# Performance work log

Measured on AMD Instinct MI355X. Metric: run time of the kernel, lower is better.

## Reference

```python
import jax, jax.numpy as jnp
import numpy as np

N_L = 100000   # local nodes
N_V = 1000     # virtual nodes
D_IN = 64
H = 64         # hidden_channels
D_OUT = 32
E_LL = 1000000
E_LV = 100000
E_VV = 50000


def setup_inputs() -> dict:
    key = jax.random.key(0)
    ks = jax.random.split(key, 16)
    s_in = 1.0 / np.sqrt(D_IN)   # fan-in init scale
    s_h = 1.0 / np.sqrt(H)
    return {
        "x_local": jax.random.normal(ks[0], (N_L, D_IN), jnp.float32),
        "x_virtual": jax.random.normal(ks[1], (N_V, D_IN), jnp.float32),
        # GCNConv (local->local): weight + bias
        "W_gcn": jax.random.normal(ks[2], (D_IN, H), jnp.float32) * s_in,
        "b_gcn": jnp.zeros((H,), jnp.float32),
        # SAGEConv (local->virtual): lin_l (neighbor agg, with bias), lin_r (root)
        "Wl_lv": jax.random.normal(ks[3], (D_IN, H), jnp.float32) * s_in,
        "Wr_lv": jax.random.normal(ks[4], (D_IN, H), jnp.float32) * s_in,
        "b_lv": jnp.zeros((H,), jnp.float32),
        # SAGEConv (virtual->virtual)
        "Wl_vv": jax.random.normal(ks[5], (D_IN, H), jnp.float32) * s_in,
        "Wr_vv": jax.random.normal(ks[6], (D_IN, H), jnp.float32) * s_in,
        "b_vv": jnp.zeros((H,), jnp.float32),
        # final Linear(hidden -> dim_out)
        "W_lin": jax.random.normal(ks[7], (H, D_OUT), jnp.float32) * s_h,
        "b_lin": jnp.zeros((D_OUT,), jnp.float32),
        # edge indices
        "edge_ll": jax.random.randint(ks[8], (2, E_LL), 0, N_L),
        "edge_lv_src": jax.random.randint(ks[9], (E_LV,), 0, N_L),
        "edge_lv_dst": jax.random.randint(ks[10], (E_LV,), 0, N_V),
        "edge_vv": jax.random.randint(ks[11], (2, E_VV), 0, N_V),
    }


def _gcn_conv(x, W, b, row, col, n):
    # gcn_norm with add_self_loops=False: deg from dst (col), sym norm
    ones = jnp.ones(row.shape[0], x.dtype)
    deg = jax.ops.segment_sum(ones, col, num_segments=n)
    dinv = jnp.where(deg > 0, jax.lax.rsqrt(jnp.maximum(deg, 1.0)), 0.0)
    norm = dinv[row] * dinv[col]                      # [E]
    h = x @ W                                         # [n,H]
    msg = h[row] * norm[:, None]                      # [E,H] gather
    return jax.ops.segment_sum(msg, col, num_segments=n) + b


def _sage_conv(x_src, x_dst, Wl, Wr, b, src, dst, n_dst):
    # mean aggregation of source features over in-edges
    agg = jax.ops.segment_sum(x_src[src], dst, num_segments=n_dst)
    cnt = jax.ops.segment_sum(jnp.ones(src.shape[0], x_src.dtype), dst,
                              num_segments=n_dst)
    agg = agg / jnp.maximum(cnt, 1.0)[:, None]
    return agg @ Wl + b + x_dst @ Wr


def reference(x_local, x_virtual, W_gcn, b_gcn, Wl_lv, Wr_lv, b_lv,
              Wl_vv, Wr_vv, b_vv, W_lin, b_lin,
              edge_ll, edge_lv_src, edge_lv_dst, edge_vv):
    # HeteroConv layer (sum-aggregate outputs per destination node type)
    out_ll = _gcn_conv(x_local, W_gcn, b_gcn, edge_ll[0], edge_ll[1], N_L)
    out_lv = _sage_conv(x_local, x_virtual, Wl_lv, Wr_lv, b_lv,
                        edge_lv_src, edge_lv_dst, N_V)
    out_vv = _sage_conv(x_virtual, x_virtual, Wl_vv, Wr_vv, b_vv,
                        edge_vv[0], edge_vv[1], N_V)
    h_local = jax.nn.relu(out_ll)
    h_virtual = jax.nn.relu(out_lv + out_vv)  # sum across relations -> relu
    del h_virtual  # only 'local' feeds the final linear head
    return h_local @ W_lin + b_lin
```

## Files before the change

### kernel.cpp

```cpp
#include <hip/hip_runtime.h>

#define N_L 100000
#define N_V 1000
#define D_IN 64
#define HCH 64
#define D_OUT 32
#define E_LL 1000000

#define NCLS 8
#define DST_PER_CLS 12500
#define NBLK1 1024
#define BCAP 256
#define GW 400
#define NSB 32
#define NGSB 256
#define SUBCAP 4608
#define SCSTRIDE 16

#define L2CAP 384
#define L2THR 128
#define BINSUB_BPC 64
#define SLABS (NBLK1 / BINSUB_BPC)

typedef unsigned int uint32;
typedef unsigned long long u64;
typedef __attribute__((ext_vector_type(8))) short bfx8;
typedef __attribute__((ext_vector_type(4))) float f32x4;
typedef __attribute__((ext_vector_type(4))) float fvec4;
typedef __attribute__((ext_vector_type(4))) unsigned short usvec4;

__device__ inline float bf2f(unsigned short u) {
    return __uint_as_float(((uint32)u) << 16);
}
__device__ inline unsigned short f2bf(float f) {
    uint32 u = __float_as_uint(f);
    u = (u + 0x7fffu + ((u >> 16) & 1u)) >> 16;
    return (unsigned short)u;
}
__device__ inline void bar_lds() {
    asm volatile("s_waitcnt lgkmcnt(0)\n\ts_barrier" ::: "memory");
}

__global__ __launch_bounds__(256) void binclass_kernel(
    const int* __restrict__ row, const int* __restrict__ col,
    int* __restrict__ classcnt, uint32* __restrict__ classpairs)
{
    __shared__ uint32 sbin[NCLS][BCAP];
    __shared__ int scnt[NCLS];
    if (threadIdx.x < NCLS) scnt[threadIdx.x] = 0;
    bar_lds();

    const int blk = blockIdx.x;
    const int per = (E_LL + NBLK1 - 1) / NBLK1;
    const int beg = blk * per;
    const int end = (beg + per < E_LL) ? beg + per : E_LL;
    const int lane = threadIdx.x & 63;
    const int wv = threadIdx.x >> 6;

    for (int i0 = beg; i0 < end; i0 += 256) {
        int i = i0 + threadIdx.x;
        if (i < end) {
            int c = col[i];
            int r = row[i];
            int cls = c / DST_PER_CLS;
            uint32 pack = ((uint32)r << 14) | (uint32)(c - cls * DST_PER_CLS);
            u64 act = __ballot(1);
            u64 b0 = __ballot(cls & 1);
            u64 b1 = __ballot(cls & 2);
            u64 b2 = __ballot(cls & 4);
            u64 mask = ((cls & 1) ? b0 : ~b0) & ((cls & 2) ? b1 : ~b1)
                     & ((cls & 4) ? b2 : ~b2) & act;
            int leader = __ffsll(mask) - 1;
            int rank = __popcll(mask & ((1ull << lane) - 1ull));
            int base = 0;
            if (lane == leader) base = atomicAdd(&scnt[cls], __popcll(mask));
            base = __shfl(base, leader);
            int slot = base + rank;
            if (slot < BCAP) sbin[cls][slot] = pack;
        }
    }
    bar_lds();
    for (int b = wv; b < NCLS; b += 4) {
        int cnt = scnt[b]; if (cnt > BCAP) cnt = BCAP;
        uint32* dst = classpairs + ((size_t)b * NBLK1 + blk) * BCAP;
        for (int k = lane; k < cnt; k += 64) dst[k] = sbin[b][k];
        if (lane == 0) classcnt[b * NBLK1 + blk] = cnt;
    }
}

__global__ __launch_bounds__(256) void binsub_kernel(
    const int* __restrict__ classcnt, const uint32* __restrict__ classpairs,
    int* __restrict__ subcur, uint32* __restrict__ subpairs)
{
    __shared__ uint32 sbin[NSB][L2CAP];
    __shared__ int scnt[NSB];
    if (threadIdx.x < NSB) scnt[threadIdx.x] = 0;
    bar_lds();

    const int cls = blockIdx.x / BINSUB_BPC;
    const int chunk = blockIdx.x % BINSUB_BPC;
    const int s0 = chunk * SLABS;
    const int lane = threadIdx.x & 63;
    const int wv = threadIdx.x >> 6;

    for (int s = s0; s < s0 + SLABS; ++s) {
        int len = classcnt[cls * NBLK1 + s];
        const uint32* cp = classpairs + ((size_t)cls * NBLK1 + s) * BCAP;
        if (threadIdx.x < len) {
            uint32 p = cp[threadIdx.x];
            int c_lo = (int)(p & 16383u);
            uint32 r = p >> 14;
            int sb = c_lo / GW;
            uint32 pack = (r << 9) | (uint32)(c_lo - sb * GW);
            u64 act = __ballot(1);
            u64 b0 = __ballot(sb & 1);
            u64 b1 = __ballot(sb & 2);
            u64 b2 = __ballot(sb & 4);
            u64 b3 = __ballot(sb & 8);
            u64 b4 = __ballot(sb & 16);
            u64 mask = ((sb & 1) ? b0 : ~b0) & ((sb & 2) ? b1 : ~b1)
                     & ((sb & 4) ? b2 : ~b2) & ((sb & 8) ? b3 : ~b3)
                     & ((sb & 16) ? b4 : ~b4) & act;
            int leader = __ffsll(mask) - 1;
            int rank = __popcll(mask & ((1ull << lane) - 1ull));
            int base = 0;
            if (lane == leader) base = atomicAdd(&scnt[sb], __popcll(mask));
            base = __shfl(base, leader);
            sbin[sb][base + rank] = pack;
        }
        bar_lds();
        for (int b = wv; b < NSB; b += 4) {
            int cnt = scnt[b];
            if (cnt >= L2THR) {
                int gb;
                int gsb = cls * NSB + b;
                if (lane == 0) gb = atomicAdd(&subcur[gsb * SCSTRIDE], cnt);
                gb = __shfl(gb, 0);
                uint32* dst = subpairs + (size_t)gsb * SUBCAP;
                for (int k = lane; k < cnt; k += 64)
                    if (gb + k < SUBCAP) dst[gb + k] = sbin[b][k];
                if (lane == 0) scnt[b] = 0;
            }
        }
        bar_lds();
    }
    for (int b = wv; b < NSB; b += 4) {
        int cnt = scnt[b];
        if (cnt > 0) {
            int gb;
            int gsb = cls * NSB + b;
            if (lane == 0) gb = atomicAdd(&subcur[gsb * SCSTRIDE], cnt);
            gb = __shfl(gb, 0);
            uint32* dst = subpairs + (size_t)gsb * SUBCAP;
            for (int k = lane; k < cnt; k += 64)
                if (gb + k < SUBCAP) dst[gb + k] = sbin[b][k];
        }
    }
}

__global__ __launch_bounds__(512) void degdinv_kernel(
    const uint32* __restrict__ subpairs, const int* __restrict__ subcur,
    float* __restrict__ dinv)
{
    __shared__ int hcnt[512];
    const int gsb = blockIdx.x;
    const int cls = gsb >> 5;
    const int sb = gsb & 31;
    const int lo = cls * DST_PER_CLS + sb * GW;
    int w = DST_PER_CLS - sb * GW; if (w > GW) w = GW;

    hcnt[threadIdx.x] = 0;
    bar_lds();
    int cnt = subcur[gsb * SCSTRIDE]; if (cnt > SUBCAP) cnt = SUBCAP;
    const uint32* sp = subpairs + (size_t)gsb * SUBCAP;
    for (int i = threadIdx.x; i < cnt; i += 512)
        atomicAdd(&hcnt[sp[i] & 511u], 1);
    bar_lds();
    if (threadIdx.x < w) {
        int d = hcnt[threadIdx.x];
        dinv[lo + threadIdx.x] = (d > 0) ? rsqrtf((float)d) : 0.0f;
    }
}

__global__ void xbconv_kernel(const float* __restrict__ x,
                              const float* __restrict__ dinv,
                              unsigned short* __restrict__ xb) {
    int n4 = N_L * D_IN / 4;
    int idx = blockIdx.x * blockDim.x + threadIdx.x;
    int stride = gridDim.x * blockDim.x;
    for (; idx < n4; idx += stride) {
        fvec4 v = ((const fvec4*)x)[idx];
        float d = dinv[idx >> 4];
        usvec4 o;
        o.x = f2bf(v.x * d);
        o.y = f2bf(v.y * d);
        o.z = f2bf(v.z * d);
        o.w = f2bf(v.w * d);
        ((usvec4*)xb)[idx] = o;
    }
}

__global__ __launch_bounds__(1024) void gather_epi_kernel(
    const unsigned short* __restrict__ xb,
    const uint32* __restrict__ subpairs, const int* __restrict__ subcur,
    const float* __restrict__ Wg, const float* __restrict__ bg,
    const float* __restrict__ Wl, const float* __restrict__ bl,
    float* __restrict__ out)
{
    extern __shared__ char smem[];
    unsigned short* hacc = (unsigned short*)smem;
    unsigned short* hbufp = (unsigned short*)(smem + 57600);
    uint32* sorted = (uint32*)(smem + 94464);
    int* rptr  = (int*)(smem + 112896);
    int* scan2 = (int*)(smem + 114944);
    int* cur   = (int*)(smem + 116992);

    const int gsb = blockIdx.x;
    const int cls = gsb >> 5;
    const int sb = gsb & 31;
    const int lo = cls * DST_PER_CLS + sb * GW;
    int w = DST_PER_CLS - sb * GW; if (w > GW) w = GW;

    const int tid = threadIdx.x;
    const int lane = tid & 63;
    const int wv = tid >> 6;

    int cnt = subcur[gsb * SCSTRIDE]; if (cnt > SUBCAP) cnt = SUBCAP;
    const uint32* sp = subpairs + (size_t)gsb * SUBCAP;

    if (tid < 512) rptr[tid] = 0;
    bar_lds();
    for (int i = tid; i < cnt; i += 1024)
        atomicAdd(&rptr[sp[i] & 511u], 1);
    bar_lds();

    int v = (tid < 512) ? rptr[tid] : 0;
    if (tid < 512) scan2[tid] = v;
    bar_lds();
    for (int ofs = 1; ofs < 512; ofs <<= 1) {
        int add = (tid < 512 && tid >= ofs) ? scan2[tid - ofs] : 0;
        bar_lds();
        if (tid < 512) scan2[tid] += add;
        bar_lds();
    }
    if (tid < 512) {
        int ex = scan2[tid] - v;
        rptr[tid] = ex;
        if (tid < 400) cur[tid] = ex;
    }
    bar_lds();

    for (int i = tid; i < cnt; i += 1024) {
        uint32 p = sp[i];
        int pos = atomicAdd(&cur[p & 511u], 1);
        sorted[pos] = p >> 9;
    }
    bar_lds();

    for (int c = wv; c < w; c += 16) {
        int s = rptr[c], e = rptr[c + 1];
        int cntc = e - s;
        float a0 = 0.f, a1 = 0.f, a2 = 0.f, a3 = 0.f;
        float a4 = 0.f, a5 = 0.f, a6 = 0.f, a7 = 0.f;
        int j = s;
        for (; j + 8 <= e; j += 8) {
            int r0 = sorted[j], r1 = sorted[j + 1];
            int r2 = sorted[j + 2], r3 = sorted[j + 3];
            int r4 = sorted[j + 4], r5 = sorted[j + 5];
            int r6 = sorted[j + 6], r7 = sorted[j + 7];
            a0 += bf2f(xb[(size_t)r0 * D_IN + lane]);
            a1 += bf2f(xb[(size_t)r1 * D_IN + lane]);
            a2 += bf2f(xb[(size_t)r2 * D_IN + lane]);
            a3 += bf2f(xb[(size_t)r3 * D_IN + lane]);
            a4 += bf2f(xb[(size_t)r4 * D_IN + lane]);
            a5 += bf2f(xb[(size_t)r5 * D_IN + lane]);
            a6 += bf2f(xb[(size_t)r6 * D_IN + lane]);
            a7 += bf2f(xb[(size_t)r7 * D_IN + lane]);
        }
        for (; j < e; ++j) {
            int r = sorted[j];
            a0 += bf2f(xb[(size_t)r * D_IN + lane]);
        }
        float dv = (cntc > 0) ? rsqrtf((float)cntc) : 0.0f;
        float s01 = (a0 + a1) + (a2 + a3);
        float s23 = (a4 + a5) + (a6 + a7);
        hacc[c * 72 + lane] = f2bf((s01 + s23) * dv);
    }
    bar_lds();

    const int lm = lane & 15, lg = lane >> 4, kseg = lg * 8;

    bfx8 wg0[4], wg1[4], wl0[2], wl1[2];
    #pragma unroll
    for (int n = 0; n < 4; ++n) {
        #pragma unroll
        for (int jj = 0; jj < 8; ++jj) {
            wg0[n][jj] = (short)f2bf(Wg[(kseg + jj) * HCH + n * 16 + lm]);
            wg1[n][jj] = (short)f2bf(Wg[(32 + kseg + jj) * HCH + n * 16 + lm]);
        }
    }
    #pragma unroll
    for (int n = 0; n < 2; ++n) {
        #pragma unroll
        for (int jj = 0; jj < 8; ++jj) {
            wl0[n][jj] = (short)f2bf(Wl[(kseg + jj) * D_OUT + n * 16 + lm]);
            wl1[n][jj] = (short)f2bf(Wl[(32 + kseg + jj) * D_OUT + n * 16 + lm]);
        }
    }
    float bgv[4], blv[2];
    #pragma unroll
    for (int n = 0; n < 4; ++n) bgv[n] = bg[n * 16 + lm];
    #pragma unroll
    for (int n = 0; n < 2; ++n) blv[n] = bl[n * 16 + lm];

    const int ntile = (w + 15) >> 4;
    for (int t = wv; t < ntile; t += 16) {
        const int m0 = t * 16;
        const int arow = m0 + lm;
        const unsigned short* fr = hacc + arow * 72;
        bfx8 a0 = *(const bfx8*)(fr + kseg);
        bfx8 a1 = *(const bfx8*)(fr + 32 + kseg);

        unsigned short* hb = hbufp + wv * (16 * 72);
        #pragma unroll
        for (int n = 0; n < 4; ++n) {
            f32x4 cacc = {0.0f, 0.0f, 0.0f, 0.0f};
            cacc = __builtin_amdgcn_mfma_f32_16x16x32_bf16(a0, wg0[n], cacc, 0, 0, 0);
            cacc = __builtin_amdgcn_mfma_f32_16x16x32_bf16(a1, wg1[n], cacc, 0, 0, 0);
            #pragma unroll
            for (int i = 0; i < 4; ++i) {
                float h = fmaxf(cacc[i] + bgv[n], 0.0f);
                hb[(lg * 4 + i) * 72 + n * 16 + lm] = f2bf(h);
            }
        }
        bfx8 a20 = *(const bfx8*)(hb + lm * 72 + kseg);
        bfx8 a21 = *(const bfx8*)(hb + lm * 72 + 32 + kseg);

        #pragma unroll
        for (int n2 = 0; n2 < 2; ++n2) {
            f32x4 d = {0.0f, 0.0f, 0.0f, 0.0f};
            d = __builtin_amdgcn_mfma_f32_16x16x32_bf16(a20, wl0[n2], d, 0, 0, 0);
            d = __builtin_amdgcn_mfma_f32_16x16x32_bf16(a21, wl1[n2], d, 0, 0, 0);
            #pragma unroll
            for (int i = 0; i < 4; ++i) {
                int mrow = m0 + lg * 4 + i;
                if (mrow < w)
                    out[(size_t)(lo + mrow) * D_OUT + n2 * 16 + lm] = d[i] + blv[n2];
            }
        }
    }
}

extern "C" void kernel_launch(void* const* d_in, const int* in_sizes, int n_in,
                              void* d_out, int out_size, void* d_ws, size_t ws_size,
                              hipStream_t stream) {
    const float* x_local = (const float*)d_in[0];
    const float* W_gcn   = (const float*)d_in[2];
    const float* b_gcn   = (const float*)d_in[3];
    const float* W_lin   = (const float*)d_in[10];
    const float* b_lin   = (const float*)d_in[11];
    const int*   edge_ll = (const int*)d_in[12];
    const int*   row = edge_ll;
    const int*   col = edge_ll + E_LL;

    char* base = (char*)d_ws;
    int*    subcur     = (int*)(base + 0);
    int*    classcnt   = (int*)(base + 16384);
    float*  dinvp      = (float*)(base + 49152);
    uint32* classpairs = (uint32*)(base + 449536);
    uint32* subpairs   = (uint32*)(base + 8838144);
    unsigned short* xb = (unsigned short*)(base + 13556736);
    float* out = (float*)d_out;

    (void)hipMemsetAsync(base, 0, 16384, stream);

    binclass_kernel<<<NBLK1, 256, 0, stream>>>(row, col, classcnt, classpairs);
    binsub_kernel<<<NCLS * BINSUB_BPC, 256, 0, stream>>>(
        classcnt, classpairs, subcur, subpairs);
    degdinv_kernel<<<NGSB, 512, 0, stream>>>(subpairs, subcur, dinvp);
    xbconv_kernel<<<2048, 256, 0, stream>>>(x_local, dinvp, xb);
    gather_epi_kernel<<<NGSB, 1024, 118592, stream>>>(
        xb, subpairs, subcur, W_gcn, b_gcn, W_lin, b_lin, out);
}
```

Before: 112.4 us.

## Split gather-epilogue into half-bin blocks and reuse precomputed row pointers

The degree kernel now also computes the per-sub-bin exclusive prefix sum and writes it to global memory. The gather-epilogue kernel is split so each 400-node bin is handled by two 512-thread blocks of 200 nodes, using about half the LDS. This drops the in-kernel histogram and scan, and the smaller blocks should improve occupancy and spread work across more CUs. In exchange, each block still scans the whole bin's pair list and keeps only the half it owns, and a new SORTCAP bound can silently drop edges if one half overflows.

```diff
diff --git a/kernel.cpp b/kernel.cpp
--- a/kernel.cpp
+++ b/kernel.cpp
@@ -12,9 +12,11 @@
 #define NBLK1 1024
 #define BCAP 256
 #define GW 400
+#define HW 200
 #define NSB 32
 #define NGSB 256
 #define SUBCAP 4608
+#define SORTCAP 2560
 #define SCSTRIDE 16
 
 #define L2CAP 384
@@ -160,26 +162,37 @@
 
 __global__ __launch_bounds__(512) void degdinv_kernel(
     const uint32* __restrict__ subpairs, const int* __restrict__ subcur,
-    float* __restrict__ dinv)
+    float* __restrict__ dinv, int* __restrict__ rptrg)
 {
     __shared__ int hcnt[512];
+    __shared__ int scn[512];
     const int gsb = blockIdx.x;
     const int cls = gsb >> 5;
     const int sb = gsb & 31;
     const int lo = cls * DST_PER_CLS + sb * GW;
     int w = DST_PER_CLS - sb * GW; if (w > GW) w = GW;
-
-    hcnt[threadIdx.x] = 0;
+    const int tid = threadIdx.x;
+
+    hcnt[tid] = 0;
     bar_lds();
     int cnt = subcur[gsb * SCSTRIDE]; if (cnt > SUBCAP) cnt = SUBCAP;
     const uint32* sp = subpairs + (size_t)gsb * SUBCAP;
-    for (int i = threadIdx.x; i < cnt; i += 512)
+    for (int i = tid; i < cnt; i += 512)
         atomicAdd(&hcnt[sp[i] & 511u], 1);
     bar_lds();
-    if (threadIdx.x < w) {
-        int d = hcnt[threadIdx.x];
-        dinv[lo + threadIdx.x] = (d > 0) ? rsqrtf((float)d) : 0.0f;
-    }
+
+    int v = hcnt[tid];
+    scn[tid] = v;
+    bar_lds();
+    for (int ofs = 1; ofs < 512; ofs <<= 1) {
+        int add = (tid >= ofs) ? scn[tid - ofs] : 0;
+        bar_lds();
+        scn[tid] += add;
+        bar_lds();
+    }
+    rptrg[gsb * 512 + tid] = scn[tid] - v;
+    if (tid < w)
+        dinv[lo + tid] = (v > 0) ? rsqrtf((float)v) : 0.0f;
 }
 
 __global__ void xbconv_kernel(const float* __restrict__ x,
@@ -200,26 +213,30 @@
     }
 }
 
-__global__ __launch_bounds__(1024) void gather_epi_kernel(
+__global__ __launch_bounds__(512) void gather_epi_kernel(
     const unsigned short* __restrict__ xb,
     const uint32* __restrict__ subpairs, const int* __restrict__ subcur,
+    const int* __restrict__ rptrg,
     const float* __restrict__ Wg, const float* __restrict__ bg,
     const float* __restrict__ Wl, const float* __restrict__ bl,
     float* __restrict__ out)
 {
     extern __shared__ char smem[];
-    unsigned short* hacc = (unsigned short*)smem;
-    unsigned short* hbufp = (unsigned short*)(smem + 57600);
-    uint32* sorted = (uint32*)(smem + 94464);
-    int* rptr  = (int*)(smem + 112896);
-    int* scan2 = (int*)(smem + 114944);
-    int* cur   = (int*)(smem + 116992);
-
-    const int gsb = blockIdx.x;
+    unsigned short* hacc  = (unsigned short*)smem;
+    unsigned short* hbufp = (unsigned short*)(smem + 29952);
+    uint32* sorted = (uint32*)(smem + 48384);
+    int* rptr_l = (int*)(smem + 58624);
+    int* cur    = (int*)(smem + 59456);
+
+    const int gsb = blockIdx.x >> 1;
+    const int hb  = blockIdx.x & 1;
     const int cls = gsb >> 5;
-    const int sb = gsb & 31;
-    const int lo = cls * DST_PER_CLS + sb * GW;
-    int w = DST_PER_CLS - sb * GW; if (w > GW) w = GW;
+    const int sb  = gsb & 31;
+    const int lo_bin = cls * DST_PER_CLS + sb * GW;
+    int wbin = DST_PER_CLS - sb * GW; if (wbin > GW) wbin = GW;
+    const int lo_node = hb * HW;
+    int w = wbin - lo_node; if (w > HW) w = HW; if (w < 0) w = 0;
+    const int lo = lo_bin + lo_node;
 
     const int tid = threadIdx.x;
     const int lane = tid & 63;
@@ -227,38 +244,29 @@
 
     int cnt = subcur[gsb * SCSTRIDE]; if (cnt > SUBCAP) cnt = SUBCAP;
     const uint32* sp = subpairs + (size_t)gsb * SUBCAP;
-
-    if (tid < 512) rptr[tid] = 0;
-    bar_lds();
-    for (int i = tid; i < cnt; i += 1024)
-        atomicAdd(&rptr[sp[i] & 511u], 1);
-    bar_lds();
-
-    int v = (tid < 512) ? rptr[tid] : 0;
-    if (tid < 512) scan2[tid] = v;
-    bar_lds();
-    for (int ofs = 1; ofs < 512; ofs <<= 1) {
-        int add = (tid < 512 && tid >= ofs) ? scan2[tid - ofs] : 0;
-        bar_lds();
-        if (tid < 512) scan2[tid] += add;
-        bar_lds();
-    }
-    if (tid < 512) {
-        int ex = scan2[tid] - v;
-        rptr[tid] = ex;
-        if (tid < 400) cur[tid] = ex;
-    }
-    bar_lds();
-
-    for (int i = tid; i < cnt; i += 1024) {
+    const int* rg = rptrg + gsb * 512;
+
+    const int base0 = rg[lo_node];
+    if (tid <= w) {
+        int rl = rg[lo_node + tid] - base0;
+        rptr_l[tid] = rl;
+        if (tid < w) cur[tid] = rl;
+    }
+    bar_lds();
+
+    for (int i = tid; i < cnt; i += 512) {
         uint32 p = sp[i];
-        int pos = atomicAdd(&cur[p & 511u], 1);
-        sorted[pos] = p >> 9;
-    }
-    bar_lds();
-
-    for (int c = wv; c < w; c += 16) {
-        int s = rptr[c], e = rptr[c + 1];
+        int cl = (int)(p & 511u) - lo_node;
+        if (cl >= 0 && cl < w) {
+            int pos = atomicAdd(&cur[cl], 1);
+            if (pos < SORTCAP) sorted[pos] = p >> 9;
+        }
+    }
+    bar_lds();
+
+    for (int c = wv; c < w; c += 8) {
+        int s = rptr_l[c], e = rptr_l[c + 1];
+        if (e > SORTCAP) e = SORTCAP;
         int cntc = e - s;
         float a0 = 0.f, a1 = 0.f, a2 = 0.f, a3 = 0.f;
         float a4 = 0.f, a5 = 0.f, a6 = 0.f, a7 = 0.f;
@@ -288,6 +296,8 @@
     }
     bar_lds();
 
+    if (w == 0) return;
+
     const int lm = lane & 15, lg = lane >> 4, kseg = lg * 8;
 
     bfx8 wg0[4], wg1[4], wl0[2], wl1[2];
@@ -314,14 +324,14 @@
     for (int n = 0; n < 2; ++n) blv[n] = bl[n * 16 + lm];
 
     const int ntile = (w + 15) >> 4;
-    for (int t = wv; t < ntile; t += 16) {
+    for (int t = wv; t < ntile; t += 8) {
         const int m0 = t * 16;
         const int arow = m0 + lm;
         const unsigned short* fr = hacc + arow * 72;
         bfx8 a0 = *(const bfx8*)(fr + kseg);
         bfx8 a1 = *(const bfx8*)(fr + 32 + kseg);
 
-        unsigned short* hb = hbufp + wv * (16 * 72);
+        unsigned short* hbw = hbufp + wv * (16 * 72);
         #pragma unroll
         for (int n = 0; n < 4; ++n) {
             f32x4 cacc = {0.0f, 0.0f, 0.0f, 0.0f};
@@ -330,11 +340,11 @@
             #pragma unroll
             for (int i = 0; i < 4; ++i) {
                 float h = fmaxf(cacc[i] + bgv[n], 0.0f);
-                hb[(lg * 4 + i) * 72 + n * 16 + lm] = f2bf(h);
+                hbw[(lg * 4 + i) * 72 + n * 16 + lm] = f2bf(h);
             }
         }
-        bfx8 a20 = *(const bfx8*)(hb + lm * 72 + kseg);
-        bfx8 a21 = *(const bfx8*)(hb + lm * 72 + 32 + kseg);
+        bfx8 a20 = *(const bfx8*)(hbw + lm * 72 + kseg);
+        bfx8 a21 = *(const bfx8*)(hbw + lm * 72 + 32 + kseg);
 
         #pragma unroll
         for (int n2 = 0; n2 < 2; ++n2) {
@@ -367,9 +377,10 @@
     int*    subcur     = (int*)(base + 0);
     int*    classcnt   = (int*)(base + 16384);
     float*  dinvp      = (float*)(base + 49152);
-    uint32* classpairs = (uint32*)(base + 449536);
-    uint32* subpairs   = (uint32*)(base + 8838144);
-    unsigned short* xb = (unsigned short*)(base + 13556736);
+    int*    rptrg      = (int*)(base + 449536);
+    uint32* classpairs = (uint32*)(base + 973824);
+    uint32* subpairs   = (uint32*)(base + 9362432);
+    unsigned short* xb = (unsigned short*)(base + 14081024);
     float* out = (float*)d_out;
 
     (void)hipMemsetAsync(base, 0, 16384, stream);
@@ -377,8 +388,8 @@
     binclass_kernel<<<NBLK1, 256, 0, stream>>>(row, col, classcnt, classpairs);
     binsub_kernel<<<NCLS * BINSUB_BPC, 256, 0, stream>>>(
         classcnt, classpairs, subcur, subpairs);
-    degdinv_kernel<<<NGSB, 512, 0, stream>>>(subpairs, subcur, dinvp);
+    degdinv_kernel<<<NGSB, 512, 0, stream>>>(subpairs, subcur, dinvp, rptrg);
     xbconv_kernel<<<2048, 256, 0, stream>>>(x_local, dinvp, xb);
-    gather_epi_kernel<<<NGSB, 1024, 118592, stream>>>(
-        xb, subpairs, subcur, W_gcn, b_gcn, W_lin, b_lin, out);
-}
+    gather_epi_kernel<<<2 * NGSB, 512, 60416, stream>>>(
+        xb, subpairs, subcur, rptrg, W_gcn, b_gcn, W_lin, b_lin, out);
+}
```

After: 112.2 us. Within noise of the previous version (-0.1%).
